# Performance work log

Measured on AMD Instinct MI355X. Metric: run time of the kernel, lower is better.

Reference implementation:

```python
import jax, jax.numpy as jnp
import numpy as np

N_NODES = 20000
N_EDGES = 320000
F = 128          # n_features
NB = 20          # n_basis (radial Bessel functions)
L = 3            # n_interactions
RC = 5.0         # cutoff radius


def setup_inputs() -> dict:
    key = jax.random.key(0)
    ks = jax.random.split(key, 16)
    s = 0.08  # ~1/sqrt(F) init scale
    z = jax.random.randint(ks[0], (N_NODES,), 1, 119)
    disp = jax.random.normal(ks[1], (N_EDGES, 3), jnp.float32) * 1.5
    edge_index = jax.random.randint(ks[2], (2, N_EDGES), 0, N_NODES)
    batch = jnp.zeros((N_NODES,), jnp.int64)
    node_emb = jax.random.normal(ks[3], (119, F), jnp.float32) * s
    node_emb = node_emb.at[0].set(0.0)  # padding_idx=0
    return {
        'z': z, 'disp': disp, 'edge_index': edge_index, 'batch': batch,
        'node_emb': node_emb,
        'mnp_W1': jax.random.normal(ks[4], (L, F, F), jnp.float32) * s,
        'mnp_b1': jnp.zeros((L, F), jnp.float32),
        'mnp_W2': jax.random.normal(ks[5], (L, F, F), jnp.float32) * s,
        'mnp_b2': jnp.zeros((L, F), jnp.float32),
        'me_W': jax.random.normal(ks[6], (L, F, NB), jnp.float32) * s,
        'eq1_W1': jax.random.normal(ks[7], (L, F, F), jnp.float32) * s,
        'eq1_W2': jax.random.normal(ks[8], (L, F, F), jnp.float32) * s,
        'eq2_W1': jax.random.normal(ks[9], (L, F, F), jnp.float32) * s,
        'eq2_W2': jax.random.normal(ks[10], (L, F, F), jnp.float32) * s,
        'upd_W': jax.random.normal(ks[11], (L, F, F), jnp.float32) * s,
    }


def _edge_embedding(disp):
    # norm -> (dist, dir); cosine cutoff * Bessel radial basis
    dist = jnp.linalg.norm(disp, axis=1)                      # [E]
    dir_edge = disp / dist[:, None]                           # [E,3]
    cut = 0.5 * (jnp.cos(jnp.pi * dist / RC) + 1.0) * (dist < RC)
    n = jnp.arange(1, NB + 1, dtype=disp.dtype)
    rbf = jnp.sqrt(2.0 / RC) * jnp.sin(n[None, :] * jnp.pi * dist[:, None] / RC) / dist[:, None]
    dist_edge = cut[:, None] * rbf                            # [E,NB]
    return dist_edge, dir_edge


def reference(z, disp, edge_index, batch, node_emb,
              mnp_W1, mnp_b1, mnp_W2, mnp_b2, me_W,
              eq1_W1, eq1_W2, eq2_W1, eq2_W2, upd_W):
    n_nodes = z.shape[0]
    dist_edge, dir_edge = _edge_embedding(disp)
    atom = node_emb[z]                                        # [N,F]
    force = jnp.zeros((n_nodes, 3, F), dist_edge.dtype)       # [N,3,F]
    ei0, ei1 = edge_index[0], edge_index[1]

    for l in range(L):
        # invariant message: edge part * node parts gathered at both ends
        mnp = jax.nn.silu(atom @ mnp_W1[l].T + mnp_b1[l]) @ mnp_W2[l].T + mnp_b2[l]
        mep = dist_edge @ me_W[l].T                           # [E,F]
        msg = mep * mnp[ei0] * mnp[ei1]                       # [E,F]
        atom = atom + jax.ops.segment_sum(msg, ei0, num_segments=n_nodes)
        # equivariant messages (outer products via broadcast)
        e1 = (jax.nn.silu(msg @ eq1_W1[l].T) @ eq1_W2[l].T)[:, None, :] * dir_edge[:, :, None]
        e2 = (jax.nn.silu(msg @ eq2_W1[l].T) @ eq2_W2[l].T)[:, None, :] * force[ei1]
        force = force + jax.ops.segment_sum(e1 + e2, ei0, num_segments=n_nodes)
        # invariant update from equivariant channel
        atom = atom + jnp.sum(force * jnp.einsum('nvf,gf->nvg', force, upd_W[l]), axis=1)

    return atom, force
```

## Files before the change

### kernel.cpp

```cpp
#include <hip/hip_runtime.h>
#include <hip/hip_bf16.h>
#include <cstdint>
#include <cstddef>

#define FDIM   128
#define NBASIS 20
#define NLAYERS 3
#define RCUT   5.0f
#define PI_F   3.14159265358979323846f
#define CHUNK  64
#define TPB    512

typedef __attribute__((ext_vector_type(8))) short bf16x8;
typedef __attribute__((ext_vector_type(4))) float f32x4;

__device__ __forceinline__ float silu_f(float x) { return x / (1.f + __expf(-x)); }

__device__ __forceinline__ unsigned short f2bf(float x) {
    __hip_bfloat16 h = __float2bfloat16(x);
    unsigned short u;
    __builtin_memcpy(&u, &h, 2);
    return u;
}

__device__ __forceinline__ int swz(int row, int col) {
    return row * FDIM + (col ^ ((row & 7) << 3));
}
__device__ __forceinline__ int swz4(int row, int col) {
    return row * FDIM + (col ^ ((row & 7) << 2));
}

__global__ __launch_bounds__(256)
void atom_init_kernel(const int* __restrict__ zc, const float* __restrict__ emb,
                      float* __restrict__ atom, int N)
{
    int t = blockIdx.x * 256 + threadIdx.x;
    if (t >= N * FDIM) return;
    int n = t >> 7, f = t & 127;
    atom[t] = emb[zc[n]*FDIM + f];
}

__global__ __launch_bounds__(256)
void zero4_kernel(float4* __restrict__ p, int n4)
{
    int t = blockIdx.x * 256 + threadIdx.x;
    if (t < n4) p[t] = make_float4(0.f,0.f,0.f,0.f);
}

__global__ __launch_bounds__(256)
void pack_w_kernel(const float* __restrict__ mnpW1, const float* __restrict__ mnpW2,
                   const float* __restrict__ e11,   const float* __restrict__ e12,
                   const float* __restrict__ e21,   const float* __restrict__ e22,
                   const float* __restrict__ updW,
                   unsigned short* __restrict__ wpk)
{
    int t = blockIdx.x * 256 + threadIdx.x;
    if (t >= 21 * 2048) return;
    int m = t >> 11, p = t & 2047;
    int layer = m / 7, kind = m % 7;
    const float* base;
    switch (kind) {
        case 0: base = mnpW1; break;
        case 1: base = mnpW2; break;
        case 2: base = e11;   break;
        case 3: base = e12;   break;
        case 4: base = e21;   break;
        case 5: base = e22;   break;
        default: base = updW; break;
    }
    base += (size_t)layer * FDIM * FDIM;
    int l   = p & 63, fr = p >> 6;
    int r16 = fr >> 2, ks = fr & 3;
    int row = r16*16 + (l & 15);
    int col = ks*32 + (l >> 4)*8;
    const float* src = base + (size_t)row*FDIM + col;
    float4 v0 = *reinterpret_cast<const float4*>(src);
    float4 v1 = *reinterpret_cast<const float4*>(src + 4);
    unsigned short* dst = wpk + (size_t)t * 8;
    ushort4 o0, o1;
    o0.x = f2bf(v0.x); o0.y = f2bf(v0.y); o0.z = f2bf(v0.z); o0.w = f2bf(v0.w);
    o1.x = f2bf(v1.x); o1.y = f2bf(v1.y); o1.z = f2bf(v1.z); o1.w = f2bf(v1.w);
    *reinterpret_cast<ushort4*>(dst)     = o0;
    *reinterpret_cast<ushort4*>(dst + 4) = o1;
}

__global__ __launch_bounds__(256)
void hist_kernel(const int* __restrict__ ei0, int* __restrict__ hist, int E)
{
    int e = blockIdx.x * 256 + threadIdx.x;
    if (e < E) atomicAdd(&hist[ei0[e]], 1);
}

__global__ __launch_bounds__(1024)
void prefix_kernel(const int* __restrict__ hist, int* __restrict__ off, int N, int E)
{
    __shared__ int buf[1024];
    __shared__ int carry;
    const int tid = threadIdx.x;
    if (tid == 0) carry = 0;
    __syncthreads();
    for (int base = 0; base < N; base += 1024) {
        int i = base + tid;
        int v = (i < N) ? hist[i] : 0;
        buf[tid] = v;
        __syncthreads();
        for (int d = 1; d < 1024; d <<= 1) {
            int t = (tid >= d) ? buf[tid - d] : 0;
            __syncthreads();
            buf[tid] += t;
            __syncthreads();
        }
        if (i < N) off[i] = carry + buf[tid] - v;
        __syncthreads();
        if (tid == 0) carry += buf[1023];
        __syncthreads();
    }
}

__global__ __launch_bounds__(256)
void scatter_kernel(const int* __restrict__ ei0, const int* __restrict__ ei1,
                    const float* __restrict__ disp, int* __restrict__ off,
                    int* __restrict__ se0, int* __restrict__ se1,
                    float* __restrict__ sdisp, int E)
{
    int e = blockIdx.x * 256 + threadIdx.x;
    if (e >= E) return;
    int n = ei0[e];
    int pos = atomicAdd(&off[n], 1);
    se0[pos] = n;
    se1[pos] = ei1[e];
    sdisp[3*pos+0] = disp[3*e+0];
    sdisp[3*pos+1] = disp[3*e+1];
    sdisp[3*pos+2] = disp[3*e+2];
}

__device__ __forceinline__ void gemm_g(const unsigned short* __restrict__ Ab,
                                       const unsigned short* __restrict__ Bpk,
                                       int mr0, int nc0, int lane, f32x4 acc[4])
{
    #pragma unroll
    for (int ks = 0; ks < 4; ++ks) {
        bf16x8 a = *reinterpret_cast<const bf16x8*>(
            &Ab[swz(mr0 + (lane & 15), ks*32 + (lane >> 4)*8)]);
        #pragma unroll
        for (int n = 0; n < 4; ++n) {
            int r16 = (nc0 >> 4) + n;
            bf16x8 b = *reinterpret_cast<const bf16x8*>(
                &Bpk[(size_t)(((r16*4 + ks)*64 + lane)) * 8]);
            acc[n] = __builtin_amdgcn_mfma_f32_16x16x32_bf16(a, b, acc[n], 0, 0, 0);
        }
    }
}

__global__ __launch_bounds__(TPB, 6)
void node_mlp_g_kernel(const float* __restrict__ in, float* __restrict__ out,
                       const unsigned short* __restrict__ W1pk, const float* __restrict__ b1,
                       const unsigned short* __restrict__ W2pk, const float* __restrict__ b2,
                       int R)
{
    __shared__ __align__(16) unsigned short Ab[CHUNK*FDIM];
    __shared__ __align__(16) unsigned short Hb[CHUNK*FDIM];
    const int tid  = threadIdx.x;
    const int lane = tid & 63;
    const int wid  = tid >> 6;
    const int r0   = blockIdx.x * CHUNK;
    const int mr0  = (wid & 3) * 16;
    const int nc0  = (wid >> 2) * 64;

    {
        const float4* g = reinterpret_cast<const float4*>(in) + (size_t)r0 * (FDIM/4);
        #pragma unroll
        for (int i = 0; i < 4; ++i) {
            int p = tid + i*TPB;
            int r = p >> 5, c4 = p & 31;
            float4 v = make_float4(0.f,0.f,0.f,0.f);
            if (r0 + r < R) v = g[p];
            ushort4 o;
            o.x = f2bf(v.x); o.y = f2bf(v.y); o.z = f2bf(v.z); o.w = f2bf(v.w);
            *reinterpret_cast<ushort4*>(&Ab[swz(r, c4*4)]) = o;
        }
    }
    __syncthreads();

    f32x4 acc[4];
    #pragma unroll
    for (int n = 0; n < 4; ++n) acc[n] = (f32x4){0.f,0.f,0.f,0.f};
    gemm_g(Ab, W1pk, mr0, nc0, lane, acc);
    #pragma unroll
    for (int n = 0; n < 4; ++n) {
        int col = nc0 + n*16 + (lane & 15);
        float bv = b1[col];
        #pragma unroll
        for (int q = 0; q < 4; ++q)
            Hb[swz(mr0 + (lane >> 4)*4 + q, col)] = f2bf(silu_f(acc[n][q] + bv));
    }
    __syncthreads();

    #pragma unroll
    for (int n = 0; n < 4; ++n) acc[n] = (f32x4){0.f,0.f,0.f,0.f};
    gemm_g(Hb, W2pk, mr0, nc0, lane, acc);
    #pragma unroll
    for (int n = 0; n < 4; ++n) {
        int col = nc0 + n*16 + (lane & 15);
        float bv = b2[col];
        #pragma unroll
        for (int q = 0; q < 4; ++q) {
            int grow = r0 + mr0 + (lane >> 4)*4 + q;
            if (grow < R) out[(size_t)grow*FDIM + col] = acc[n][q] + bv;
        }
    }
}

__global__ __launch_bounds__(TPB, 6)
void edge_layer_kernel(const float* __restrict__ sdisp,
                       const int* __restrict__ se0, const int* __restrict__ se1,
                       const float* __restrict__ mnp,
                       const float* __restrict__ meW,
                       const unsigned short* __restrict__ W11pk,
                       const unsigned short* __restrict__ W12pk,
                       const unsigned short* __restrict__ W21pk,
                       const unsigned short* __restrict__ W22pk,
                       const float* __restrict__ fold,
                       float* __restrict__ atom,
                       float* __restrict__ fnew,
                       int E)
{
    __shared__ __align__(16) union {
        struct { unsigned short Ab[CHUNK*FDIM]; unsigned short Hb0[CHUNK*FDIM]; } g;
        float S[CHUNK*FDIM];
    } U;
    __shared__ __align__(16) union {
        unsigned short Hb1[CHUNK*FDIM];
        float de[CHUNK][NBASIS];
    } V;
    __shared__ float dirc[CHUNK][3];
    __shared__ int   e0c[CHUNK], e1c[CHUNK];
    __shared__ int   segrow[CHUNK];
    __shared__ int   nseg_sh;

    const int tid  = threadIdx.x;
    const int lane = tid & 63;
    const int wid  = tid >> 6;
    const int r0   = blockIdx.x * CHUNK;
    const int nvalid = min(CHUNK, E - r0);
    const int mr0  = (wid & 3) * 16;
    const int nc0  = (wid >> 2) * 64;

    if (tid < CHUNK) {
        int r = tid;
        int gidx  = r0 + min(r, nvalid - 1);
        int gprev = r0 + min(r - 1, nvalid - 1);
        int e0v = se0[gidx];
        bool head = (r == 0) || (r < nvalid && se0[gprev] != e0v);
        e0c[r] = e0v;
        int a1i = 0;
        float x = 0.f, y = 0.f, zz = 0.f;
        if (r < nvalid) {
            a1i = se1[r0 + r];
            const float* dp = sdisp + 3*(size_t)(r0 + r);
            x = dp[0]; y = dp[1]; zz = dp[2];
        }
        e1c[r] = a1i;
        float d   = sqrtf(x*x + y*y + zz*zz);
        float inv = (r < nvalid) ? 1.0f/d : 0.f;
        dirc[r][0] = x*inv; dirc[r][1] = y*inv; dirc[r][2] = zz*inv;
        float w   = PI_F * d / RCUT;
        float cut = (d < RCUT) ? 0.5f*(cosf(w) + 1.f) : 0.f;
        float coef = sqrtf(2.f/RCUT) * cut * inv;
        float s1 = sinf(w);
        float c2 = 2.f * cosf(w);
        V.de[r][0] = coef * s1;
        float sm2 = 0.f, sm1 = s1;
        #pragma unroll
        for (int nn = 2; nn <= NBASIS; ++nn) {
            float sn = c2*sm1 - sm2;
            V.de[r][nn-1] = coef * sn;
            sm2 = sm1; sm1 = sn;
        }
        unsigned long long mask = __ballot(head);
        int sid = __popcll(mask & ((1ULL << r) - 1ULL));
        if (head) segrow[sid] = r;
        if (r == 0) nseg_sh = (int)__popcll(mask);
    }
    __syncthreads();

    {
        const int f  = tid & 127;
        const int q4 = tid >> 7;
        float mew[NBASIS];
        #pragma unroll
        for (int b = 0; b < NBASIS; ++b) mew[b] = meW[(size_t)f*NBASIS + b];
        float m1v[16];
        #pragma unroll
        for (int i = 0; i < 16; ++i)
            m1v[i] = mnp[(size_t)e1c[q4*16 + i]*FDIM + f];
        int   prev = e0c[q4*16];
        float mv0  = mnp[(size_t)prev*FDIM + f];
        float macc = 0.f;
        #pragma unroll
        for (int i = 0; i < 16; ++i) {
            int r = q4*16 + i;
            int e0 = e0c[r];
            if (e0 != prev) {
                atomicAdd(&atom[(size_t)prev*FDIM + f], macc);
                macc = 0.f; prev = e0;
                mv0 = mnp[(size_t)e0*FDIM + f];
            }
            float m = 0.f;
            if (r < nvalid) {
                float mep = 0.f;
                #pragma unroll
                for (int b = 0; b < NBASIS; ++b) mep += V.de[r][b] * mew[b];
                m = mep * mv0 * m1v[i];
                macc += m;
            }
            U.g.Ab[swz(r, f)] = f2bf(m);
        }
        atomicAdd(&atom[(size_t)prev*FDIM + f], macc);
    }
    __syncthreads();

    f32x4 va1[4], va2[4];

    #pragma unroll
    for (int n = 0; n < 4; ++n) va1[n] = (f32x4){0.f,0.f,0.f,0.f};
    gemm_g(U.g.Ab, W11pk, mr0, nc0, lane, va1);
    #pragma unroll
    for (int n = 0; n < 4; ++n)
        #pragma unroll
        for (int q = 0; q < 4; ++q)
            U.g.Hb0[swz(mr0 + (lane >> 4)*4 + q, nc0 + n*16 + (lane & 15))] =
                f2bf(silu_f(va1[n][q]));

    #pragma unroll
    for (int n = 0; n < 4; ++n) va2[n] = (f32x4){0.f,0.f,0.f,0.f};
    gemm_g(U.g.Ab, W21pk, mr0, nc0, lane, va2);
    #pragma unroll
    for (int n = 0; n < 4; ++n)
        #pragma unroll
        for (int q = 0; q < 4; ++q)
            V.Hb1[swz(mr0 + (lane >> 4)*4 + q, nc0 + n*16 + (lane & 15))] =
                f2bf(silu_f(va2[n][q]));
    __syncthreads();

    #pragma unroll
    for (int n = 0; n < 4; ++n) va1[n] = (f32x4){0.f,0.f,0.f,0.f};
    gemm_g(U.g.Hb0, W12pk, mr0, nc0, lane, va1);
    #pragma unroll
    for (int n = 0; n < 4; ++n) va2[n] = (f32x4){0.f,0.f,0.f,0.f};
    gemm_g(V.Hb1, W22pk, mr0, nc0, lane, va2);
    __syncthreads();

    const int nseg = nseg_sh;
    for (int v = 0; v < 3; ++v) {
        #pragma unroll
        for (int q = 0; q < 4; ++q) {
            int row = mr0 + (lane >> 4)*4 + q;
            const float* fb = fold + (size_t)e1c[row]*3*FDIM + v*FDIM;
            float dv = dirc[row][v];
            #pragma unroll
            for (int n = 0; n < 4; ++n) {
                int col = nc0 + n*16 + (lane & 15);
                U.S[swz4(row, col)] = va1[n][q]*dv + va2[n][q]*fb[col];
            }
        }
        __syncthreads();
        {
            int col = tid & 127;
            for (int s = tid >> 7; s < nseg; s += 4) {
                int rb = segrow[s];
                int re = (s + 1 < nseg) ? segrow[s+1] : CHUNK;
                float sum = 0.f;
                for (int r = rb; r < re; ++r) sum += U.S[swz4(r, col)];
                atomicAdd(&fnew[(size_t)e0c[rb]*3*FDIM + v*FDIM + col], sum);
            }
        }
        __syncthreads();
    }
}

__global__ __launch_bounds__(TPB, 6)
void upd_mfma_kernel(const float* __restrict__ fc, const unsigned short* __restrict__ Wpk,
                     float* __restrict__ atom, float* __restrict__ fcopy, int R)
{
    __shared__ __align__(16) unsigned short Ab[CHUNK*FDIM];
    const int tid  = threadIdx.x;
    const int lane = tid & 63;
    const int wid  = tid >> 6;
    const int r0   = blockIdx.x * CHUNK;
    const int mr0  = (wid & 3) * 16;
    const int nc0  = (wid >> 2) * 64;

    {
        const float4* g = reinterpret_cast<const float4*>(fc) + (size_t)r0 * (FDIM/4);
        float4*      cp = fcopy ? reinterpret_cast<float4*>(fcopy) + (size_t)r0 * (FDIM/4)
                                : nullptr;
        #pragma unroll
        for (int i = 0; i < 4; ++i) {
            int p = tid + i*TPB;
            int r = p >> 5, c4 = p & 31;
            float4 v = make_float4(0.f,0.f,0.f,0.f);
            if (r0 + r < R) {
                v = g[p];
                if (cp) cp[p] = v;
            }
            ushort4 o;
            o.x = f2bf(v.x); o.y = f2bf(v.y); o.z = f2bf(v.z); o.w = f2bf(v.w);
            *reinterpret_cast<ushort4*>(&Ab[swz(r, c4*4)]) = o;
        }
    }
    __syncthreads();

    f32x4 acc[4];
    #pragma unroll
    for (int n = 0; n < 4; ++n) acc[n] = (f32x4){0.f,0.f,0.f,0.f};
    gemm_g(Ab, Wpk, mr0, nc0, lane, acc);

    #pragma unroll
    for (int n = 0; n < 4; ++n)
        #pragma unroll
        for (int q = 0; q < 4; ++q) {
            int row  = mr0 + (lane >> 4)*4 + q;
            int col  = nc0 + n*16 + (lane & 15);
            int grow = r0 + row;
            if (grow < R) {
                float fv = fc[(size_t)grow*FDIM + col];
                atomicAdd(&atom[(size_t)(grow/3)*FDIM + col], acc[n][q] * fv);
            }
        }
}

extern "C" void kernel_launch(void* const* d_in, const int* in_sizes, int n_in,
                              void* d_out, int out_size, void* d_ws, size_t ws_size,
                              hipStream_t stream)
{
    const int*   zc    = (const int*)d_in[0];
    const float* disp  = (const float*)d_in[1];
    const int*   ei    = (const int*)d_in[2];
    const float* emb   = (const float*)d_in[4];
    const float* mnpW1 = (const float*)d_in[5];
    const float* mnpb1 = (const float*)d_in[6];
    const float* mnpW2 = (const float*)d_in[7];
    const float* mnpb2 = (const float*)d_in[8];
    const float* meW   = (const float*)d_in[9];
    const float* eq1W1 = (const float*)d_in[10];
    const float* eq1W2 = (const float*)d_in[11];
    const float* eq2W1 = (const float*)d_in[12];
    const float* eq2W2 = (const float*)d_in[13];
    const float* updW  = (const float*)d_in[14];

    const int N = in_sizes[0];
    const int E = in_sizes[1] / 3;
    const int* ei0 = ei;
    const int* ei1 = ei + E;

    float* atom = (float*)d_out;
    float* fB   = (float*)d_out + (size_t)N * FDIM;

    float* ws   = (float*)d_ws;
    float* mnp   = ws;  ws += (size_t)N * FDIM;
    float* fA    = ws;  ws += (size_t)N * 3 * FDIM;
    float* sdisp = ws;  ws += (size_t)E * 3;
    unsigned short* wpk = (unsigned short*)ws;
    ws = (float*)(wpk + (size_t)21 * FDIM * FDIM);
    int*   hist  = (int*)ws;
    int*   off   = hist + N;
    int*   se0   = off + N + 1;
    int*   se1   = se0 + E;

    const int n4F3 = N * 3 * FDIM / 4;
    const int eb   = (E + 255) / 256;
    const size_t MS = (size_t)FDIM * FDIM;

    pack_w_kernel<<<(21*2048 + 255)/256, 256, 0, stream>>>(
        mnpW1, mnpW2, eq1W1, eq1W2, eq2W1, eq2W2, updW, wpk);
    hipMemsetAsync(hist, 0, (size_t)N * sizeof(int), stream);
    hist_kernel<<<eb, 256, 0, stream>>>(ei0, hist, E);
    prefix_kernel<<<1, 1024, 0, stream>>>(hist, off, N, E);
    scatter_kernel<<<eb, 256, 0, stream>>>(ei0, ei1, disp, off, se0, se1, sdisp, E);

    atom_init_kernel<<<(N*FDIM + 255)/256, 256, 0, stream>>>(zc, emb, atom, N);
    zero4_kernel<<<(n4F3 + 255)/256, 256, 0, stream>>>((float4*)fA, n4F3);

    for (int l = 0; l < NLAYERS; ++l) {
        const float* fold;  float* fnew;
        if      (l == 0) { fold = fA; fnew = fB; }
        else if (l == 1) { fold = fB; fnew = fA; }
        else             { fold = fA; fnew = fB; }

        const unsigned short* Lpk = wpk + (size_t)l * 7 * MS;

        node_mlp_g_kernel<<<(N + CHUNK - 1)/CHUNK, TPB, 0, stream>>>(
            atom, mnp,
            Lpk + 0*MS, mnpb1 + (size_t)l*FDIM,
            Lpk + 1*MS, mnpb2 + (size_t)l*FDIM, N);

        if (l == 0) zero4_kernel<<<(n4F3 + 255)/256, 256, 0, stream>>>((float4*)fnew, n4F3);

        edge_layer_kernel<<<(E + CHUNK - 1)/CHUNK, TPB, 0, stream>>>(
            sdisp, se0, se1, mnp,
            meW + (size_t)l*FDIM*NBASIS,
            Lpk + 2*MS, Lpk + 3*MS, Lpk + 4*MS, Lpk + 5*MS,
            fold, atom, fnew, E);

        upd_mfma_kernel<<<(3*N + CHUNK - 1)/CHUNK, TPB, 0, stream>>>(
            fnew, Lpk + 6*MS, atom,
            (l < NLAYERS-1) ? (float*)fold : nullptr, 3*N);
    }
}
```

Measured before the change: 824.2 us.

## Shrink edge-kernel LDS by sharing one hidden buffer and raise occupancy bounds

Removes the second shared hidden buffer from the edge kernel. The two equivariant MLP branches are now run one after another through a single shared Hb region, which is unioned with the padded radial-basis table, so LDS per block drops. Launch bounds go from 6 to 8 blocks per CU on three kernels, SiLU uses a hardware reciprocal, and the radial-basis dot product is vectorised with float4. In exchange the edge kernel gains extra barriers and serialises the branches, and the tighter register budget may cause spills.

```diff
diff --git a/kernel.cpp b/kernel.cpp
--- a/kernel.cpp
+++ b/kernel.cpp
@@ -14,7 +14,9 @@
 typedef __attribute__((ext_vector_type(8))) short bf16x8;
 typedef __attribute__((ext_vector_type(4))) float f32x4;
 
-__device__ __forceinline__ float silu_f(float x) { return x / (1.f + __expf(-x)); }
+__device__ __forceinline__ float silu_f(float x) {
+    return x * __builtin_amdgcn_rcpf(1.f + __expf(-x));
+}
 
 __device__ __forceinline__ unsigned short f2bf(float x) {
     __hip_bfloat16 h = __float2bfloat16(x);
@@ -152,7 +154,7 @@
     }
 }
 
-__global__ __launch_bounds__(TPB, 6)
+__global__ __launch_bounds__(TPB, 8)
 void node_mlp_g_kernel(const float* __restrict__ in, float* __restrict__ out,
                        const unsigned short* __restrict__ W1pk, const float* __restrict__ b1,
                        const unsigned short* __restrict__ W2pk, const float* __restrict__ b2,
@@ -211,7 +213,7 @@
     }
 }
 
-__global__ __launch_bounds__(TPB, 6)
+__global__ __launch_bounds__(TPB, 8)
 void edge_layer_kernel(const float* __restrict__ sdisp,
                        const int* __restrict__ se0, const int* __restrict__ se1,
                        const float* __restrict__ mnp,
@@ -225,14 +227,16 @@
                        float* __restrict__ fnew,
                        int E)
 {
-    __shared__ __align__(16) union {
-        struct { unsigned short Ab[CHUNK*FDIM]; unsigned short Hb0[CHUNK*FDIM]; } g;
+    __shared__ __align__(16) union UU {
+        struct GG {
+            unsigned short Ab[CHUNK*FDIM];
+            union HH {
+                unsigned short Hb[CHUNK*FDIM];
+                float de[CHUNK][24];
+            } h;
+        } g;
         float S[CHUNK*FDIM];
     } U;
-    __shared__ __align__(16) union {
-        unsigned short Hb1[CHUNK*FDIM];
-        float de[CHUNK][NBASIS];
-    } V;
     __shared__ float dirc[CHUNK][3];
     __shared__ int   e0c[CHUNK], e1c[CHUNK];
     __shared__ int   segrow[CHUNK];
@@ -269,12 +273,12 @@
         float coef = sqrtf(2.f/RCUT) * cut * inv;
         float s1 = sinf(w);
         float c2 = 2.f * cosf(w);
-        V.de[r][0] = coef * s1;
+        U.g.h.de[r][0] = coef * s1;
         float sm2 = 0.f, sm1 = s1;
         #pragma unroll
         for (int nn = 2; nn <= NBASIS; ++nn) {
             float sn = c2*sm1 - sm2;
-            V.de[r][nn-1] = coef * sn;
+            U.g.h.de[r][nn-1] = coef * sn;
             sm2 = sm1; sm1 = sn;
         }
         unsigned long long mask = __ballot(head);
@@ -287,13 +291,17 @@
     {
         const int f  = tid & 127;
         const int q4 = tid >> 7;
-        float mew[NBASIS];
-        #pragma unroll
-        for (int b = 0; b < NBASIS; ++b) mew[b] = meW[(size_t)f*NBASIS + b];
         float m1v[16];
         #pragma unroll
         for (int i = 0; i < 16; ++i)
             m1v[i] = mnp[(size_t)e1c[q4*16 + i]*FDIM + f];
+        float4 mw[5];
+        {
+            const float* wr = meW + (size_t)f*NBASIS;
+            #pragma unroll
+            for (int k = 0; k < 5; ++k)
+                mw[k] = make_float4(wr[4*k], wr[4*k+1], wr[4*k+2], wr[4*k+3]);
+        }
         int   prev = e0c[q4*16];
         float mv0  = mnp[(size_t)prev*FDIM + f];
         float macc = 0.f;
@@ -308,9 +316,13 @@
             }
             float m = 0.f;
             if (r < nvalid) {
+                const float4* der = reinterpret_cast<const float4*>(&U.g.h.de[r][0]);
                 float mep = 0.f;
                 #pragma unroll
-                for (int b = 0; b < NBASIS; ++b) mep += V.de[r][b] * mew[b];
+                for (int k = 0; k < 5; ++k) {
+                    float4 d = der[k];
+                    mep += d.x*mw[k].x + d.y*mw[k].y + d.z*mw[k].z + d.w*mw[k].w;
+                }
                 m = mep * mv0 * m1v[i];
                 macc += m;
             }
@@ -320,35 +332,38 @@
     }
     __syncthreads();
 
-    f32x4 va1[4], va2[4];
+    f32x4 va1[4], va2[4], vt[4];
+
+    #pragma unroll
+    for (int n = 0; n < 4; ++n) vt[n] = (f32x4){0.f,0.f,0.f,0.f};
+    gemm_g(U.g.Ab, W11pk, mr0, nc0, lane, vt);
+    #pragma unroll
+    for (int n = 0; n < 4; ++n)
+        #pragma unroll
+        for (int q = 0; q < 4; ++q)
+            U.g.h.Hb[swz(mr0 + (lane >> 4)*4 + q, nc0 + n*16 + (lane & 15))] =
+                f2bf(silu_f(vt[n][q]));
+    __syncthreads();
 
     #pragma unroll
     for (int n = 0; n < 4; ++n) va1[n] = (f32x4){0.f,0.f,0.f,0.f};
-    gemm_g(U.g.Ab, W11pk, mr0, nc0, lane, va1);
+    gemm_g(U.g.h.Hb, W12pk, mr0, nc0, lane, va1);
+    #pragma unroll
+    for (int n = 0; n < 4; ++n) vt[n] = (f32x4){0.f,0.f,0.f,0.f};
+    gemm_g(U.g.Ab, W21pk, mr0, nc0, lane, vt);
+    __syncthreads();
+
     #pragma unroll
     for (int n = 0; n < 4; ++n)
         #pragma unroll
         for (int q = 0; q < 4; ++q)
-            U.g.Hb0[swz(mr0 + (lane >> 4)*4 + q, nc0 + n*16 + (lane & 15))] =
-                f2bf(silu_f(va1[n][q]));
+            U.g.h.Hb[swz(mr0 + (lane >> 4)*4 + q, nc0 + n*16 + (lane & 15))] =
+                f2bf(silu_f(vt[n][q]));
+    __syncthreads();
 
     #pragma unroll
     for (int n = 0; n < 4; ++n) va2[n] = (f32x4){0.f,0.f,0.f,0.f};
-    gemm_g(U.g.Ab, W21pk, mr0, nc0, lane, va2);
-    #pragma unroll
-    for (int n = 0; n < 4; ++n)
-        #pragma unroll
-        for (int q = 0; q < 4; ++q)
-            V.Hb1[swz(mr0 + (lane >> 4)*4 + q, nc0 + n*16 + (lane & 15))] =
-                f2bf(silu_f(va2[n][q]));
-    __syncthreads();
-
-    #pragma unroll
-    for (int n = 0; n < 4; ++n) va1[n] = (f32x4){0.f,0.f,0.f,0.f};
-    gemm_g(U.g.Hb0, W12pk, mr0, nc0, lane, va1);
-    #pragma unroll
-    for (int n = 0; n < 4; ++n) va2[n] = (f32x4){0.f,0.f,0.f,0.f};
-    gemm_g(V.Hb1, W22pk, mr0, nc0, lane, va2);
+    gemm_g(U.g.h.Hb, W22pk, mr0, nc0, lane, va2);
     __syncthreads();
 
     const int nseg = nseg_sh;
@@ -379,7 +394,7 @@
     }
 }
 
-__global__ __launch_bounds__(TPB, 6)
+__global__ __launch_bounds__(TPB, 8)
 void upd_mfma_kernel(const float* __restrict__ fc, const unsigned short* __restrict__ Wpk,
                      float* __restrict__ atom, float* __restrict__ fcopy, int R)
 {
```

Result: slower. 1.114 ms (+35.2%).
